# Kernel tuning notes

Hardware: AMD Instinct MI355X
Metric: run time of the kernel (lower is better)

The kernel has to match this reference:

```python
import jax, jax.numpy as jnp
from jax import lax
import numpy as np

B, D, H, W = 1, 20, 96, 96
N = B * (D - 4) * H * W  # one 7x7x7 guide patch per output voxel
DN = ('NCDHW', 'OIDHW', 'NCDHW')


def _conv3(x, w, b):
    # Conv3d(1,1,kernel=3,stride=1,VALID) + bias
    y = lax.conv_general_dilated(x, w, (1, 1, 1), 'VALID', dimension_numbers=DN)
    return y + b[None, :, None, None, None]


def _guide_branch(x, w1, b1, w2, b2):
    # nn.Sequential(Conv3d, ReLU, Conv3d, ReLU): 7^3 -> 5^3 -> 3^3
    return jax.nn.relu(_conv3(jax.nn.relu(_conv3(x, w1, b1)), w2, b2))


def setup_inputs() -> dict:
    key = jax.random.key(0)
    ks = jax.random.split(key, 12)
    s = 1.0 / np.sqrt(27.0)  # torch Conv3d default init scale (fan_in = 1*3*3*3)
    return {
        'x': jax.random.normal(ks[0], (B, 1, D, H, W), jnp.float32),
        'domain_neighbor': jax.random.uniform(ks[1], (1, 1, 7, 7, 7), jnp.float32),
        'guide_im': jax.random.normal(ks[2], (N, 1, 7, 7, 7), jnp.float32),
        'w1_d': jax.random.normal(ks[3], (1, 1, 3, 3, 3), jnp.float32) * s,
        'b1_d': jax.random.normal(ks[4], (1,), jnp.float32) * s,
        'w2_d': jax.random.normal(ks[5], (1, 1, 3, 3, 3), jnp.float32) * s,
        'b2_d': jax.random.normal(ks[6], (1,), jnp.float32) * s,
        'w1_r': jax.random.normal(ks[7], (1, 1, 3, 3, 3), jnp.float32) * s,
        'b1_r': jax.random.normal(ks[8], (1,), jnp.float32) * s,
        'w2_r': jax.random.normal(ks[9], (1, 1, 3, 3, 3), jnp.float32) * s,
        'b2_r': jax.random.normal(ks[10], (1,), jnp.float32) * s,
    }


def reference(x, domain_neighbor, guide_im, w1_d, b1_d, w2_d, b2_d,
              w1_r, b1_r, w2_r, b2_r):
    Bx, _, Dx, Hx, Wx = x.shape
    # kernel-generating guide nets
    domain_kernel = _guide_branch(domain_neighbor, w1_d, b1_d, w2_d, b2_d)  # (1,1,3,3,3)
    range_kernel = _guide_branch(guide_im, w1_r, b1_r, w2_r, b2_r)          # (N,1,3,3,3)
    weights = (domain_kernel * range_kernel + 1e-10).reshape(-1, 27)        # (N,27)
    # pad H,W by 1 (depth unpadded), extract all 3x3x3 patches (feature order d,h,w)
    xp = jnp.pad(x, ((0, 0), (0, 0), (0, 0), (1, 1), (1, 1)))
    p = lax.conv_general_dilated_patches(xp, (3, 3, 3), (1, 1, 1), 'VALID',
                                         dimension_numbers=DN)  # (B,27,D-2,H,W)
    p = p[:, :, 1:-1]  # keep the D-4 center-aligned depth windows (matches mat_size)
    p = p.transpose(0, 2, 3, 4, 1).reshape(-1, 27)  # (N,27)
    out = jnp.sum(weights * p, axis=1) / jnp.sum(weights, axis=1)  # weighted local mean
    return out.reshape(Bx, 1, Dx - 4, Hx, Wx)
```

## Files before the change

kernel.cpp:

```cpp
#include <hip/hip_runtime.h>
#include <hip/hip_fp16.h>


#define NPATCH 147456
#define TPB     256
#define PPB      64
#define NBLK   (NPATCH / PPB)
#define ROW_H     8
#define PATCH_H 392
#define PATCH_D 196
#define NROWS  (PPB * 49)

typedef float f4u __attribute__((ext_vector_type(4), aligned(4)));
typedef float f2u __attribute__((ext_vector_type(2), aligned(4)));

__global__ __launch_bounds__(128) void domain_branch_kernel(
    const float* __restrict__ dn,
    const float* __restrict__ w1, const float* __restrict__ b1,
    const float* __restrict__ w2, const float* __restrict__ b2,
    float* __restrict__ dom_out)
{
    __shared__ float s_in[344];
    __shared__ float s_c1[128];
    const int t = threadIdx.x;
    for (int idx = t; idx < 343; idx += 128) s_in[idx] = dn[idx];
    __syncthreads();
    if (t < 125) {
        const int i = t / 25, j = (t / 5) % 5, k = t % 5;
        float acc = b1[0];
        const float* base = &s_in[i * 49 + j * 7 + k];
#pragma unroll
        for (int dz = 0; dz < 3; ++dz)
#pragma unroll
            for (int dy = 0; dy < 3; ++dy)
#pragma unroll
                for (int dx = 0; dx < 3; ++dx)
                    acc = fmaf(base[dz * 49 + dy * 7 + dx], w1[dz * 9 + dy * 3 + dx], acc);
        s_c1[t] = fmaxf(acc, 0.f);
    }
    __syncthreads();
    if (t < 27) {
        const int dz = t / 9, dy = (t / 3) % 3, dx = t % 3;
        float acc = b2[0];
#pragma unroll
        for (int u = 0; u < 3; ++u)
#pragma unroll
            for (int v = 0; v < 3; ++v)
#pragma unroll
                for (int q = 0; q < 3; ++q)
                    acc = fmaf(s_c1[(dz + u) * 25 + (dy + v) * 5 + (dx + q)],
                               w2[u * 9 + v * 3 + q], acc);
        dom_out[t] = fmaxf(acc, 0.f);
    }
}

__device__ __forceinline__ float h2f_lo(unsigned int q) {
    return __half2float(__ushort_as_half((unsigned short)(q & 0xffffu)));
}
__device__ __forceinline__ float h2f_hi(unsigned int q) {
    return __half2float(__ushort_as_half((unsigned short)(q >> 16)));
}
__device__ __forceinline__ unsigned int pkh(float lo, float hi) {
    return __builtin_bit_cast(unsigned int, __builtin_amdgcn_cvt_pkrtz(lo, hi));
}

__device__ __forceinline__ void load_row(const unsigned int* __restrict__ P, float* d,
                                         int zi, int y) {
    const int d0 = zi * 28 + y * 4;
    const uint4 q = *reinterpret_cast<const uint4*>(P + d0);
    d[0] = h2f_lo(q.x); d[1] = h2f_hi(q.x);
    d[2] = h2f_lo(q.y); d[3] = h2f_hi(q.y);
    d[4] = h2f_lo(q.z); d[5] = h2f_hi(q.z);
    d[6] = h2f_lo(q.w);
}

template<int IB, int JB, int IE, int JE>
__device__ __forceinline__ void run_tasks(const unsigned int* __restrict__ P,
                                          const float* __restrict__ w1, float bb1,
                                          const float* __restrict__ w2,
                                          float (&a2)[3][3][3])
{
#pragma unroll
    for (int i = IB; i <= IE; ++i) {
        float rw[3][3][7];
        const int j0 = (i == IB) ? JB : 0;
        const int j1 = (i == IE) ? JE : 4;
#pragma unroll
        for (int j = j0; j <= j1; ++j) {
            if (j == j0) {
#pragma unroll
                for (int u = 0; u < 3; ++u)
#pragma unroll
                    for (int dy = 0; dy < 3; ++dy)
                        load_row(P, rw[u][(j + dy) % 3], i + u, j + dy);
            } else {
#pragma unroll
                for (int u = 0; u < 3; ++u)
                    load_row(P, rw[u][(j + 2) % 3], i + u, j + 2);
            }

            float c1r[5];
#pragma unroll
            for (int k = 0; k < 5; ++k) {
                float a = bb1;
#pragma unroll
                for (int u = 0; u < 3; ++u)
#pragma unroll
                    for (int v = 0; v < 3; ++v) {
                        const float* rr = rw[u][(j + v) % 3];
#pragma unroll
                        for (int w = 0; w < 3; ++w)
                            a = fmaf(rr[k + w], w1[u * 9 + v * 3 + w], a);
                    }
                c1r[k] = fmaxf(a, 0.f);
            }

#pragma unroll
            for (int dz2 = 0; dz2 < 3; ++dz2) {
                const int u2 = i - dz2;
                if (u2 >= 0 && u2 < 3) {
#pragma unroll
                    for (int v2 = 0; v2 < 3; ++v2) {
                        const int dy2 = j - v2;
                        if (dy2 >= 0 && dy2 < 3) {
#pragma unroll
                            for (int dx2 = 0; dx2 < 3; ++dx2)
#pragma unroll
                                for (int q = 0; q < 3; ++q)
                                    a2[dz2][dy2][dx2] =
                                        fmaf(c1r[dx2 + q],
                                             w2[u2 * 9 + v2 * 3 + q],
                                             a2[dz2][dy2][dx2]);
                        }
                    }
                }
            }
        }
    }
}

__global__ __launch_bounds__(TPB, 2) void jbf_main_kernel(
    const float* __restrict__ guide, const float* __restrict__ x,
    const float* __restrict__ w1, const float* __restrict__ b1,
    const float* __restrict__ w2, const float* __restrict__ b2,
    const float* __restrict__ dom, float* __restrict__ out)
{
    union SM {
        unsigned short tile[PPB * PATCH_H];
        float part[3][PPB][27];
    };
    __shared__ SM sm;

    const int tid  = threadIdx.x;
    const int wid  = tid >> 6;
    const int lane = tid & 63;
    const int blk  = blockIdx.x;

    {
        const float* __restrict__ srcf = guide + (size_t)blk * (PPB * 343);
        unsigned int* __restrict__ tdw = reinterpret_cast<unsigned int*>(sm.tile);

        int idx = tid;
        int cp = idx / 49, cr = idx - cp * 49;
        f4u a = *reinterpret_cast<const f4u*>(srcf + cp * 343 + cr * 7);
        f2u b = *reinterpret_cast<const f2u*>(srcf + cp * 343 + cr * 7 + 4);
        float c = srcf[cp * 343 + cr * 7 + 6];

#pragma unroll 1
        for (int rd = 0; rd < 12; ++rd) {
            int nidx = idx + TPB;
            if (nidx > NROWS - 1) nidx = NROWS - 1;
            const int np = nidx / 49, nr = nidx - np * 49;
            const float* s = srcf + np * 343 + nr * 7;
            f4u na = *reinterpret_cast<const f4u*>(s);
            f2u nb = *reinterpret_cast<const f2u*>(s + 4);
            float nc = s[6];

            uint4 q;
            q.x = pkh(a.x, a.y); q.y = pkh(a.z, a.w);
            q.z = pkh(b.x, b.y); q.w = pkh(c, 0.f);
            *reinterpret_cast<uint4*>(tdw + cp * PATCH_D + cr * 4) = q;

            idx = nidx; cp = np; cr = nr; a = na; b = nb; c = nc;
        }
        if (tid < NROWS - 12 * TPB) {
            uint4 q;
            q.x = pkh(a.x, a.y); q.y = pkh(a.z, a.w);
            q.z = pkh(b.x, b.y); q.w = pkh(c, 0.f);
            *reinterpret_cast<uint4*>(tdw + cp * PATCH_D + cr * 4) = q;
        }
    }
    __syncthreads();

    const unsigned int* __restrict__ P =
        reinterpret_cast<const unsigned int*>(sm.tile) + lane * PATCH_D;
    const float bb1 = b1[0];

    float a2[3][3][3];
    {
        const float init = (wid == 0) ? b2[0] : 0.f;
#pragma unroll
        for (int a = 0; a < 3; ++a)
#pragma unroll
            for (int b = 0; b < 3; ++b)
#pragma unroll
                for (int c = 0; c < 3; ++c) a2[a][b][c] = init;
    }

    if      (wid == 0) run_tasks<0, 0, 1, 1>(P, w1, bb1, w2, a2);
    else if (wid == 1) run_tasks<1, 2, 2, 3>(P, w1, bb1, w2, a2);
    else if (wid == 2) run_tasks<2, 4, 3, 4>(P, w1, bb1, w2, a2);
    else               run_tasks<4, 0, 4, 4>(P, w1, bb1, w2, a2);

    __syncthreads();

    if (wid != 0) {
#pragma unroll
        for (int t = 0; t < 27; ++t)
            sm.part[wid - 1][lane][t] = a2[t / 9][(t / 3) % 3][t % 3];
    }
    __syncthreads();

    if (wid == 0) {
        const int n   = blk * PPB + lane;
        const int dd  = n / 9216;
        const int rem = n - dd * 9216;
        const int h   = rem / 96;
        const int w_  = rem - h * 96;

        float num = 0.f, den = 0.f;
#pragma unroll
        for (int dz = 0; dz < 3; ++dz)
#pragma unroll
            for (int dy = 0; dy < 3; ++dy)
#pragma unroll
                for (int dx = 0; dx < 3; ++dx) {
                    const int t = dz * 9 + dy * 3 + dx;
                    const float r2 = fmaxf(a2[dz][dy][dx] + sm.part[0][lane][t]
                                           + sm.part[1][lane][t]
                                           + sm.part[2][lane][t], 0.f);
                    const float wt = fmaf(dom[t], r2, 1e-10f);
                    const int yy = h - 1 + dy, xx = w_ - 1 + dx;
                    float xv = 0.f;
                    if (yy >= 0 && yy < 96 && xx >= 0 && xx < 96)
                        xv = x[(dd + 1 + dz) * 9216 + yy * 96 + xx];
                    num = fmaf(wt, xv, num);
                    den += wt;
                }
        out[n] = num / den;
    }
}

extern "C" void kernel_launch(void* const* d_in, const int* in_sizes, int n_in,
                              void* d_out, int out_size, void* d_ws, size_t ws_size,
                              hipStream_t stream) {
    const float* x     = (const float*)d_in[0];
    const float* dn    = (const float*)d_in[1];
    const float* guide = (const float*)d_in[2];
    const float* w1_d  = (const float*)d_in[3];
    const float* b1_d  = (const float*)d_in[4];
    const float* w2_d  = (const float*)d_in[5];
    const float* b2_d  = (const float*)d_in[6];
    const float* w1_r  = (const float*)d_in[7];
    const float* b1_r  = (const float*)d_in[8];
    const float* w2_r  = (const float*)d_in[9];
    const float* b2_r  = (const float*)d_in[10];
    float* out = (float*)d_out;
    float* dom = (float*)d_ws;

    domain_branch_kernel<<<1, 128, 0, stream>>>(dn, w1_d, b1_d, w2_d, b2_d, dom);
    jbf_main_kernel<<<NBLK, TPB, 0, stream>>>(guide, x, w1_r, b1_r, w2_r,
                                              b2_r, dom, out);
}
```

Baseline: 52.80 us.

## Prefetch LDS rows ahead, hoist x loads early, raise occupancy bound

The row loop now loads the next packed fp16 row from LDS one iteration ahead and unpacks it later, so LDS latency overlaps the conv FMAs. Wave 0 fetches its 27 x-neighbourhood values from global memory at kernel start, before the guide tile is staged, so that latency hides behind the rest of the kernel. Launch bounds change from 2 to 3 blocks per SIMD to allow more resident waves. The costs are higher register pressure from the 27 held x values and the prefetch buffers, under a tighter register cap, which could cause spills.

```diff
diff --git a/kernel.cpp b/kernel.cpp
--- a/kernel.cpp
+++ b/kernel.cpp
@@ -64,10 +64,11 @@
     return __builtin_bit_cast(unsigned int, __builtin_amdgcn_cvt_pkrtz(lo, hi));
 }
 
-__device__ __forceinline__ void load_row(const unsigned int* __restrict__ P, float* d,
+__device__ __forceinline__ uint4 load_pk(const unsigned int* __restrict__ P,
                                          int zi, int y) {
-    const int d0 = zi * 28 + y * 4;
-    const uint4 q = *reinterpret_cast<const uint4*>(P + d0);
+    return *reinterpret_cast<const uint4*>(P + zi * 28 + y * 4);
+}
+__device__ __forceinline__ void unpack_row(const uint4 q, float* d) {
     d[0] = h2f_lo(q.x); d[1] = h2f_hi(q.x);
     d[2] = h2f_lo(q.y); d[3] = h2f_hi(q.y);
     d[4] = h2f_lo(q.z); d[5] = h2f_hi(q.z);
@@ -82,21 +83,24 @@
 {
 #pragma unroll
     for (int i = IB; i <= IE; ++i) {
-        float rw[3][3][7];
         const int j0 = (i == IB) ? JB : 0;
         const int j1 = (i == IE) ? JE : 4;
+        float rw[3][3][7];
+        uint4 pk[3];
+#pragma unroll
+        for (int u = 0; u < 3; ++u) unpack_row(load_pk(P, i + u, j0), rw[u][j0 % 3]);
+#pragma unroll
+        for (int u = 0; u < 3; ++u) unpack_row(load_pk(P, i + u, j0 + 1), rw[u][(j0 + 1) % 3]);
+#pragma unroll
+        for (int u = 0; u < 3; ++u) pk[u] = load_pk(P, i + u, j0 + 2);
+
 #pragma unroll
         for (int j = j0; j <= j1; ++j) {
-            if (j == j0) {
-#pragma unroll
-                for (int u = 0; u < 3; ++u)
-#pragma unroll
-                    for (int dy = 0; dy < 3; ++dy)
-                        load_row(P, rw[u][(j + dy) % 3], i + u, j + dy);
-            } else {
-#pragma unroll
-                for (int u = 0; u < 3; ++u)
-                    load_row(P, rw[u][(j + 2) % 3], i + u, j + 2);
+#pragma unroll
+            for (int u = 0; u < 3; ++u) unpack_row(pk[u], rw[u][(j + 2) % 3]);
+            if (j < j1) {
+#pragma unroll
+                for (int u = 0; u < 3; ++u) pk[u] = load_pk(P, i + u, j + 3);
             }
 
             float c1r[5];
@@ -139,7 +143,7 @@
     }
 }
 
-__global__ __launch_bounds__(TPB, 2) void jbf_main_kernel(
+__global__ __launch_bounds__(TPB, 3) void jbf_main_kernel(
     const float* __restrict__ guide, const float* __restrict__ x,
     const float* __restrict__ w1, const float* __restrict__ b1,
     const float* __restrict__ w2, const float* __restrict__ b2,
@@ -155,6 +159,27 @@
     const int wid  = tid >> 6;
     const int lane = tid & 63;
     const int blk  = blockIdx.x;
+    const int n    = blk * PPB + lane;
+
+    float xv[27];
+    if (wid == 0) {
+        const int dd  = n / 9216;
+        const int rem = n - dd * 9216;
+        const int h   = rem / 96;
+        const int w_  = rem - h * 96;
+#pragma unroll
+        for (int dz = 0; dz < 3; ++dz)
+#pragma unroll
+            for (int dy = 0; dy < 3; ++dy)
+#pragma unroll
+                for (int dx = 0; dx < 3; ++dx) {
+                    const int yy = h - 1 + dy, xx = w_ - 1 + dx;
+                    float v = 0.f;
+                    if (yy >= 0 && yy < 96 && xx >= 0 && xx < 96)
+                        v = x[(dd + 1 + dz) * 9216 + yy * 96 + xx];
+                    xv[dz * 9 + dy * 3 + dx] = v;
+                }
+    }
 
     {
         const float* __restrict__ srcf = guide + (size_t)blk * (PPB * 343);
@@ -222,31 +247,17 @@
     __syncthreads();
 
     if (wid == 0) {
-        const int n   = blk * PPB + lane;
-        const int dd  = n / 9216;
-        const int rem = n - dd * 9216;
-        const int h   = rem / 96;
-        const int w_  = rem - h * 96;
-
         float num = 0.f, den = 0.f;
 #pragma unroll
-        for (int dz = 0; dz < 3; ++dz)
-#pragma unroll
-            for (int dy = 0; dy < 3; ++dy)
-#pragma unroll
-                for (int dx = 0; dx < 3; ++dx) {
-                    const int t = dz * 9 + dy * 3 + dx;
-                    const float r2 = fmaxf(a2[dz][dy][dx] + sm.part[0][lane][t]
-                                           + sm.part[1][lane][t]
-                                           + sm.part[2][lane][t], 0.f);
-                    const float wt = fmaf(dom[t], r2, 1e-10f);
-                    const int yy = h - 1 + dy, xx = w_ - 1 + dx;
-                    float xv = 0.f;
-                    if (yy >= 0 && yy < 96 && xx >= 0 && xx < 96)
-                        xv = x[(dd + 1 + dz) * 9216 + yy * 96 + xx];
-                    num = fmaf(wt, xv, num);
-                    den += wt;
-                }
+        for (int t = 0; t < 27; ++t) {
+            const float r2 = fmaxf(a2[t / 9][(t / 3) % 3][t % 3]
+                                   + sm.part[0][lane][t]
+                                   + sm.part[1][lane][t]
+                                   + sm.part[2][lane][t], 0.f);
+            const float wt = fmaf(dom[t], r2, 1e-10f);
+            num = fmaf(wt, xv[t], num);
+            den += wt;
+        }
         out[n] = num / den;
     }
 }
```

Measured after the change: 53.52 us. About the same (+1.4%).

## Replace per-wave templated task bodies with table-driven segment loop for occupancy

Applied to the files above, without the earlier changes.

The four wave-specialized template instantiations of the conv1/conv2 task loop are replaced by one shared loop driven by a segment table read through readfirstlane. The sliding 3-row register window is dropped, so every c1 row reloads its nine LDS rows, and the w2 weights for the depth slice are hoisted into registers once per segment. Launch bounds go from 2 to 3 blocks per SM to raise occupancy. The cost is more LDS reads and runtime predication on J and vz instead of fully specialized code, in exchange for lower register pressure and smaller code.

```diff
diff --git a/kernel.cpp b/kernel.cpp
--- a/kernel.cpp
+++ b/kernel.cpp
@@ -63,83 +63,21 @@
 __device__ __forceinline__ unsigned int pkh(float lo, float hi) {
     return __builtin_bit_cast(unsigned int, __builtin_amdgcn_cvt_pkrtz(lo, hi));
 }
-
-__device__ __forceinline__ void load_row(const unsigned int* __restrict__ P, float* d,
-                                         int zi, int y) {
-    const int d0 = zi * 28 + y * 4;
-    const uint4 q = *reinterpret_cast<const uint4*>(P + d0);
+__device__ __forceinline__ void unpack7(const uint4 q, float* d) {
     d[0] = h2f_lo(q.x); d[1] = h2f_hi(q.x);
     d[2] = h2f_lo(q.y); d[3] = h2f_hi(q.y);
     d[4] = h2f_lo(q.z); d[5] = h2f_hi(q.z);
     d[6] = h2f_lo(q.w);
 }
 
-template<int IB, int JB, int IE, int JE>
-__device__ __forceinline__ void run_tasks(const unsigned int* __restrict__ P,
-                                          const float* __restrict__ w1, float bb1,
-                                          const float* __restrict__ w2,
-                                          float (&a2)[3][3][3])
-{
-#pragma unroll
-    for (int i = IB; i <= IE; ++i) {
-        float rw[3][3][7];
-        const int j0 = (i == IB) ? JB : 0;
-        const int j1 = (i == IE) ? JE : 4;
-#pragma unroll
-        for (int j = j0; j <= j1; ++j) {
-            if (j == j0) {
-#pragma unroll
-                for (int u = 0; u < 3; ++u)
-#pragma unroll
-                    for (int dy = 0; dy < 3; ++dy)
-                        load_row(P, rw[u][(j + dy) % 3], i + u, j + dy);
-            } else {
-#pragma unroll
-                for (int u = 0; u < 3; ++u)
-                    load_row(P, rw[u][(j + 2) % 3], i + u, j + 2);
-            }
-
-            float c1r[5];
-#pragma unroll
-            for (int k = 0; k < 5; ++k) {
-                float a = bb1;
-#pragma unroll
-                for (int u = 0; u < 3; ++u)
-#pragma unroll
-                    for (int v = 0; v < 3; ++v) {
-                        const float* rr = rw[u][(j + v) % 3];
-#pragma unroll
-                        for (int w = 0; w < 3; ++w)
-                            a = fmaf(rr[k + w], w1[u * 9 + v * 3 + w], a);
-                    }
-                c1r[k] = fmaxf(a, 0.f);
-            }
-
-#pragma unroll
-            for (int dz2 = 0; dz2 < 3; ++dz2) {
-                const int u2 = i - dz2;
-                if (u2 >= 0 && u2 < 3) {
-#pragma unroll
-                    for (int v2 = 0; v2 < 3; ++v2) {
-                        const int dy2 = j - v2;
-                        if (dy2 >= 0 && dy2 < 3) {
-#pragma unroll
-                            for (int dx2 = 0; dx2 < 3; ++dx2)
-#pragma unroll
-                                for (int q = 0; q < 3; ++q)
-                                    a2[dz2][dy2][dx2] =
-                                        fmaf(c1r[dx2 + q],
-                                             w2[u2 * 9 + v2 * 3 + q],
-                                             a2[dz2][dy2][dx2]);
-                        }
-                    }
-                }
-            }
-        }
-    }
-}
-
-__global__ __launch_bounds__(TPB, 2) void jbf_main_kernel(
+__device__ const int seg_tab[8][3] = {
+    {0, 0, 4}, {1, 0, 1},
+    {1, 2, 4}, {2, 0, 3},
+    {2, 4, 4}, {3, 0, 4},
+    {4, 0, 4}, {0, 9, 0},
+};
+
+__global__ __launch_bounds__(TPB, 3) void jbf_main_kernel(
     const float* __restrict__ guide, const float* __restrict__ x,
     const float* __restrict__ w1, const float* __restrict__ b1,
     const float* __restrict__ w2, const float* __restrict__ b2,
@@ -155,6 +93,7 @@
     const int wid  = tid >> 6;
     const int lane = tid & 63;
     const int blk  = blockIdx.x;
+    const int n    = blk * PPB + lane;
 
     {
         const float* __restrict__ srcf = guide + (size_t)blk * (PPB * 343);
@@ -207,10 +146,69 @@
                 for (int c = 0; c < 3; ++c) a2[a][b][c] = init;
     }
 
-    if      (wid == 0) run_tasks<0, 0, 1, 1>(P, w1, bb1, w2, a2);
-    else if (wid == 1) run_tasks<1, 2, 2, 3>(P, w1, bb1, w2, a2);
-    else if (wid == 2) run_tasks<2, 4, 3, 4>(P, w1, bb1, w2, a2);
-    else               run_tasks<4, 0, 4, 4>(P, w1, bb1, w2, a2);
+#pragma unroll 1
+    for (int s = 0; s < 2; ++s) {
+        const int ti = __builtin_amdgcn_readfirstlane(seg_tab[wid * 2 + s][0]);
+        const int j0 = __builtin_amdgcn_readfirstlane(seg_tab[wid * 2 + s][1]);
+        const int j1 = __builtin_amdgcn_readfirstlane(seg_tab[wid * 2 + s][2]);
+
+        float w2r[3][9];
+        bool  vz[3];
+#pragma unroll
+        for (int dz2 = 0; dz2 < 3; ++dz2) {
+            const int u2 = ti - dz2;
+            vz[dz2] = (u2 >= 0) && (u2 <= 2);
+            const int ub = (u2 < 0) ? 0 : ((u2 > 2) ? 2 : u2);
+#pragma unroll
+            for (int m = 0; m < 9; ++m) w2r[dz2][m] = w2[ub * 9 + m];
+        }
+
+        const unsigned int* __restrict__ Pi = P + ti * 28;
+
+#pragma unroll
+        for (int J = 0; J <= 4; ++J) {
+            if (J >= j0 && J <= j1) {
+                float c1r[5] = {bb1, bb1, bb1, bb1, bb1};
+#pragma unroll
+                for (int u = 0; u < 3; ++u)
+#pragma unroll
+                    for (int v = 0; v < 3; ++v) {
+                        const uint4 q = *reinterpret_cast<const uint4*>(
+                            Pi + u * 28 + (J + v) * 4);
+                        float d[7];
+                        unpack7(q, d);
+#pragma unroll
+                        for (int k = 0; k < 5; ++k)
+#pragma unroll
+                            for (int w = 0; w < 3; ++w)
+                                c1r[k] = fmaf(d[k + w], w1[u * 9 + v * 3 + w],
+                                              c1r[k]);
+                    }
+#pragma unroll
+                for (int k = 0; k < 5; ++k) c1r[k] = fmaxf(c1r[k], 0.f);
+
+#pragma unroll
+                for (int dz2 = 0; dz2 < 3; ++dz2) {
+                    if (vz[dz2]) {
+#pragma unroll
+                        for (int v2 = 0; v2 < 3; ++v2) {
+                            const int dy2 = J - v2;
+                            if (dy2 >= 0 && dy2 < 3) {
+#pragma unroll
+                                for (int dx2 = 0; dx2 < 3; ++dx2)
+#pragma unroll
+                                    for (int q = 0; q < 3; ++q)
+                                        a2[dz2][dy2][dx2] =
+                                            fmaf(c1r[dx2 + q],
+                                                 w2r[dz2][v2 * 3 + q],
+                                                 a2[dz2][dy2][dx2]);
+                            }
+                        }
+                    }
+                }
+            }
+        }
+    }
 
     __syncthreads();
 
@@ -222,7 +220,6 @@
     __syncthreads();
 
     if (wid == 0) {
-        const int n   = blk * PPB + lane;
         const int dd  = n / 9216;
         const int rem = n - dd * 9216;
         const int h   = rem / 96;
```

New measurement: 56.14 us. 6.3% more time.
